# Kernel tuning notes

Measured on AMD Instinct MI355X. Metric: run time of the kernel, lower is better.

The kernel has to match this reference:

```python
import jax, jax.numpy as jnp
import numpy as np

N_NODES = 100000
N_EDGES = 1600000
HID = 64
BN_EPS = 1e-5


def _glorot(key, shape):
    fan_in, fan_out = shape[0], shape[1]
    lim = np.sqrt(6.0 / (fan_in + fan_out))
    return jax.random.uniform(key, shape, jnp.float32, -lim, lim)


def setup_inputs() -> dict:
    key = jax.random.key(0)
    ks = jax.random.split(key, 16)
    inp = {
        "x": jax.random.normal(ks[0], (N_NODES, HID), jnp.float32),
        "edge_index": jax.random.randint(ks[1], (2, N_EDGES), 0, N_NODES, jnp.int64),
        "edge_attr": jax.random.normal(ks[2], (N_EDGES,), jnp.float32),
    }
    # per-layer GIN MLP params: Linear(in,hid) -> BN(hid) -> ReLU -> Linear(hid,out)
    for i in range(2):
        inp[f"W1_{i}"] = _glorot(ks[3 + 5 * i], (HID, HID))
        inp[f"b1_{i}"] = jnp.zeros((HID,), jnp.float32)
        inp[f"gamma_{i}"] = jnp.ones((HID,), jnp.float32)
        inp[f"beta_{i}"] = jnp.zeros((HID,), jnp.float32)
        inp[f"W2_{i}"] = _glorot(ks[4 + 5 * i], (HID, HID))
        inp[f"b2_{i}"] = jnp.zeros((HID,), jnp.float32)
    inp["Wjk"] = _glorot(ks[14], (3 * HID, HID))
    inp["bjk"] = jnp.zeros((HID,), jnp.float32)
    return inp


def _gin_conv(x, src, dst, W1, b1, gamma, beta, W2, b2):
    # GIN aggregation: (1 + eps) * x + sum_{j->i} x_j, eps = 0
    agg = jax.ops.segment_sum(x[src], dst, num_segments=N_NODES)  # [N, d]
    h = (x + agg) @ W1 + b1
    # BatchNorm1d over node dimension (training-style batch statistics)
    mean = jnp.mean(h, axis=0)
    var = jnp.var(h, axis=0)
    h = gamma * (h - mean) * jax.lax.rsqrt(var + BN_EPS) + beta
    h = jax.nn.relu(h)
    return h @ W2 + b2


def reference(x, edge_index, edge_attr,
              W1_0, b1_0, gamma_0, beta_0, W2_0, b2_0,
              W1_1, b1_1, gamma_1, beta_1, W2_1, b2_1,
              Wjk, bjk):
    # edge_attr is accepted but ignored (torch_geometric GINConv does not use it)
    src, dst = edge_index[0], edge_index[1]
    xs = [x]
    h = x
    params = [(W1_0, b1_0, gamma_0, beta_0, W2_0, b2_0),
              (W1_1, b1_1, gamma_1, beta_1, W2_1, b2_1)]
    for p in params:
        h = _gin_conv(h, src, dst, *p)
        h = jax.nn.relu(h)  # dropout p=0.0 is identity
        xs.append(h)
    return jnp.concatenate(xs, axis=-1) @ Wjk + bjk
```

## Files before the change

### kernel.cpp

```cpp
#include <hip/hip_runtime.h>

#define N_NODES 100000
#define N_EDGES 1600000
#define HID 64
#define BN_EPS 1e-5f

#define GATHER_BLOCKS (N_NODES / 32)

#define ROW_TILES (N_NODES / 16)
#define TPW1 4
#define G1_BLOCKS ((ROW_TILES + 4*TPW1 - 1) / (4*TPW1))
#define TPW2 2
#define G2_BLOCKS ((ROW_TILES + 4*TPW2 - 1) / (4*TPW2))

#define NB 391
#define MS_BLOCKS 1000
#define MS_EPB (N_EDGES / MS_BLOCKS)
#define MS_CNT (NB * MS_BLOCKS)
#define GS_CHUNK 512
#define GS_BLOCKS ((MS_CNT + GS_CHUNK - 1) / GS_CHUNK)

typedef __bf16 bf16x8 __attribute__((ext_vector_type(8)));
typedef float  f32x4  __attribute__((ext_vector_type(4)));
typedef unsigned short u16x8 __attribute__((ext_vector_type(8)));

__device__ __forceinline__ float bf2f(unsigned short u) {
    return __uint_as_float(((unsigned)u) << 16);
}
__device__ __forceinline__ unsigned short f2bf_rne(float f) {
    unsigned u = __float_as_uint(f);
    u += 0x7FFFu + ((u >> 16) & 1u);
    return (unsigned short)(u >> 16);
}

__global__ __launch_bounds__(256) void cvt_bf16_kernel(
        const float* __restrict__ in, unsigned short* __restrict__ out) {
    size_t i = ((size_t)blockIdx.x * 256 + threadIdx.x) * 8;
    if (i >= (size_t)N_NODES * HID) return;
    float4 a = *reinterpret_cast<const float4*>(in + i);
    float4 b = *reinterpret_cast<const float4*>(in + i + 4);
    ushort4 w0 = make_ushort4(f2bf_rne(a.x), f2bf_rne(a.y), f2bf_rne(a.z), f2bf_rne(a.w));
    ushort4 w1 = make_ushort4(f2bf_rne(b.x), f2bf_rne(b.y), f2bf_rne(b.z), f2bf_rne(b.w));
    *reinterpret_cast<ushort4*>(out + i) = w0;
    *reinterpret_cast<ushort4*>(out + i + 4) = w1;
}

__global__ __launch_bounds__(256) void wtrans_all_kernel(
        const float* __restrict__ Wjk,
        const float* __restrict__ W1_0, const float* __restrict__ W2_0,
        const float* __restrict__ W1_1, const float* __restrict__ W2_1,
        unsigned short* __restrict__ wjk_t,
        unsigned short* __restrict__ w1t_0, unsigned short* __restrict__ w2t_0,
        unsigned short* __restrict__ w1t_1, unsigned short* __restrict__ w2t_1) {
    int i = blockIdx.x * 256 + threadIdx.x;
    if (i < 12288) {
        int c = i / 192, k = i - c * 192;
        wjk_t[i] = f2bf_rne(Wjk[k * 64 + c]);
    } else if (i < 12288 + 16384) {
        int r = i - 12288;
        int which = r >> 12, rem = r & 4095;
        int c = rem >> 6, k = rem & 63;
        const float* W = (which == 0) ? W1_0 : (which == 1) ? W2_0
                       : (which == 2) ? W1_1 : W2_1;
        unsigned short* Wt = (which == 0) ? w1t_0 : (which == 1) ? w2t_0
                           : (which == 2) ? w1t_1 : w2t_1;
        Wt[rem] = f2bf_rne(W[k * 64 + c]);
    }
}

__global__ __launch_bounds__(256) void msplit_hist_kernel(
        const int* __restrict__ dst, int* __restrict__ cnt) {
    __shared__ int h[NB];
    for (int i = threadIdx.x; i < NB; i += 256) h[i] = 0;
    __syncthreads();
    const int e0 = blockIdx.x * MS_EPB;
    for (int e = e0 + threadIdx.x; e < e0 + MS_EPB; e += 256)
        atomicAdd(&h[dst[e] >> 8], 1);
    __syncthreads();
    for (int i = threadIdx.x; i < NB; i += 256)
        cnt[i * MS_BLOCKS + blockIdx.x] = h[i];
}

__global__ __launch_bounds__(256) void scan_partial_g(
        const int* __restrict__ in, int* __restrict__ out,
        int* __restrict__ bsums, int n) {
    __shared__ int sd[256];
    int t = threadIdx.x;
    int base = blockIdx.x * GS_CHUNK;
    int i0 = base + 2 * t, i1 = i0 + 1;
    int d0 = (i0 < n) ? in[i0] : 0;
    int d1 = (i1 < n) ? in[i1] : 0;
    sd[t] = d0 + d1;
    __syncthreads();
    for (int o = 1; o < 256; o <<= 1) {
        int v = (t >= o) ? sd[t - o] : 0;
        __syncthreads();
        sd[t] += v;
        __syncthreads();
    }
    int excl = sd[t] - (d0 + d1);
    if (i0 < n) out[i0] = excl;
    if (i1 < n) out[i1] = excl + d0;
    if (t == 255) bsums[blockIdx.x] = sd[255];
}

__global__ __launch_bounds__(256) void scan_bsums_kernel(int* __restrict__ bsums, int nb) {
    __shared__ int sd[256];
    int t = threadIdx.x;
    int v[4]; int s = 0;
#pragma unroll
    for (int k = 0; k < 4; ++k) {
        int i = t * 4 + k;
        v[k] = (i < nb) ? bsums[i] : 0;
        s += v[k];
    }
    sd[t] = s;
    __syncthreads();
    for (int o = 1; o < 256; o <<= 1) {
        int u = (t >= o) ? sd[t - o] : 0;
        __syncthreads();
        sd[t] += u;
        __syncthreads();
    }
    int run = sd[t] - s;
#pragma unroll
    for (int k = 0; k < 4; ++k) {
        int i = t * 4 + k;
        if (i < nb) bsums[i] = run;
        run += v[k];
    }
}

__global__ __launch_bounds__(256) void scan_addback_g(
        int* __restrict__ out, const int* __restrict__ bsums, int n, int total) {
    int t = threadIdx.x;
    int b = bsums[blockIdx.x];
    int base = blockIdx.x * GS_CHUNK;
    int i0 = base + 2 * t, i1 = i0 + 1;
    if (i0 < n) out[i0] += b;
    if (i1 < n) out[i1] += b;
    if (blockIdx.x == 0 && t == 0) out[n] = total;
}

__global__ __launch_bounds__(256) void msplit_scatter_kernel(
        const int* __restrict__ src, const int* __restrict__ dst,
        const int* __restrict__ psum, int* __restrict__ bucketed) {
    __shared__ int cur[NB];
    for (int i = threadIdx.x; i < NB; i += 256)
        cur[i] = psum[i * MS_BLOCKS + blockIdx.x];
    __syncthreads();
    const int e0 = blockIdx.x * MS_EPB;
    for (int e = e0 + threadIdx.x; e < e0 + MS_EPB; e += 256) {
        int d = dst[e];
        int p = atomicAdd(&cur[d >> 8], 1);
        bucketed[p] = (src[e] << 8) | (d & 255);
    }
}

__global__ __launch_bounds__(256) void bucket_csr_kernel(
        const int* __restrict__ bucketed, const int* __restrict__ psum,
        int* __restrict__ off, int* __restrict__ eidx) {
    const int j = blockIdx.x;
    const int t = threadIdx.x;
    __shared__ int deg[256];
    __shared__ int sd[256];
    __shared__ int base_s, size_s;
    if (t == 0) {
        int b = psum[j * MS_BLOCKS];
        int nxt = (j == NB - 1) ? N_EDGES : psum[(j + 1) * MS_BLOCKS];
        base_s = b; size_s = nxt - b;
    }
    deg[t] = 0;
    __syncthreads();
    const int base = base_s, size = size_s;
    const int nlo = j << 8;
    for (int i = t; i < size; i += 256)
        atomicAdd(&deg[(unsigned)bucketed[base + i] & 255u], 1);
    __syncthreads();
    int d0 = deg[t];
    sd[t] = d0;
    __syncthreads();
    for (int o = 1; o < 256; o <<= 1) {
        int v = (t >= o) ? sd[t - o] : 0;
        __syncthreads();
        sd[t] += v;
        __syncthreads();
    }
    int excl = sd[t] - d0;
    int g0 = nlo + t;
    if (g0 <= N_NODES) off[g0] = base + excl;
    __syncthreads();
    deg[t] = excl;
    __syncthreads();
    for (int i = t; i < size; i += 256) {
        unsigned e = (unsigned)bucketed[base + i];
        int p = atomicAdd(&deg[e & 255u], 1);
        eidx[base + p] = (int)(e >> 8);
    }
}

__global__ __launch_bounds__(256) void gather_kernel(
        const unsigned short* __restrict__ xb, const int* __restrict__ off,
        const int* __restrict__ eidx, unsigned short* __restrict__ aggb) {
    const int lane = threadIdx.x & 63;
    const int g    = lane >> 3;
    const int col  = (lane & 7) << 3;
    const int w    = threadIdx.x >> 6;
    const int n = blockIdx.x * 32 + w * 8 + g;

    const int beg = off[n], end = off[n + 1];
    bf16x8 s8 = *reinterpret_cast<const bf16x8*>(xb + (size_t)n * HID + col);
    float acc[8];
#pragma unroll
    for (int i = 0; i < 8; ++i) acc[i] = (float)s8[i];

    int j = beg;
    for (; j + 2 <= end; j += 2) {
        int s0 = eidx[j], s1 = eidx[j + 1];
        bf16x8 r0 = *reinterpret_cast<const bf16x8*>(xb + (size_t)s0 * HID + col);
        bf16x8 r1 = *reinterpret_cast<const bf16x8*>(xb + (size_t)s1 * HID + col);
#pragma unroll
        for (int i = 0; i < 8; ++i) acc[i] += (float)r0[i] + (float)r1[i];
    }
    if (j < end) {
        int s0 = eidx[j];
        bf16x8 r0 = *reinterpret_cast<const bf16x8*>(xb + (size_t)s0 * HID + col);
#pragma unroll
        for (int i = 0; i < 8; ++i) acc[i] += (float)r0[i];
    }

    u16x8 o;
#pragma unroll
    for (int i = 0; i < 8; ++i) o[i] = f2bf_rne(acc[i]);
    *reinterpret_cast<u16x8*>(aggb + (size_t)n * HID + col) = o;
}

__global__ __launch_bounds__(256) void gemm1_mfma_kernel(
        const unsigned short* __restrict__ aggb, const unsigned short* __restrict__ W1t,
        const float* __restrict__ bias, unsigned short* __restrict__ hb,
        float* __restrict__ stats_partial) {
    const int lane = threadIdx.x & 63;
    const int l15 = lane & 15, lhi = lane >> 4;
    const int w = threadIdx.x >> 6;

    bf16x8 bfrag[2][4];
    float bs[4];
#pragma unroll
    for (int f = 0; f < 4; ++f) {
        const unsigned short* wp = W1t + (size_t)(f * 16 + l15) * 64 + lhi * 8;
        bfrag[0][f] = *reinterpret_cast<const bf16x8*>(wp);
        bfrag[1][f] = *reinterpret_cast<const bf16x8*>(wp + 32);
        bs[f] = bias[f * 16 + l15];
    }

    float ssum[4] = {0.f, 0.f, 0.f, 0.f}, ssq[4] = {0.f, 0.f, 0.f, 0.f};

    const int tile0 = (blockIdx.x * 4 + w) * TPW1;
#pragma unroll
    for (int tt = 0; tt < TPW1; ++tt) {
        const int tile = tile0 + tt;
        if (tile < ROW_TILES) {
            const int r0 = tile * 16;
            const size_t arow = (size_t)(r0 + l15) * 64 + lhi * 8;
            bf16x8 a0 = *reinterpret_cast<const bf16x8*>(aggb + arow);
            bf16x8 a1 = *reinterpret_cast<const bf16x8*>(aggb + arow + 32);
            f32x4 acc[4];
#pragma unroll
            for (int f = 0; f < 4; ++f) acc[f] = (f32x4){bs[f], bs[f], bs[f], bs[f]};
#pragma unroll
            for (int f = 0; f < 4; ++f) {
                acc[f] = __builtin_amdgcn_mfma_f32_16x16x32_bf16(a0, bfrag[0][f], acc[f], 0, 0, 0);
                acc[f] = __builtin_amdgcn_mfma_f32_16x16x32_bf16(a1, bfrag[1][f], acc[f], 0, 0, 0);
            }
#pragma unroll
            for (int f = 0; f < 4; ++f)
#pragma unroll
                for (int i = 0; i < 4; ++i) {
                    hb[(size_t)(r0 + lhi * 4 + i) * 64 + f * 16 + l15] = f2bf_rne(acc[f][i]);
                    ssum[f] += acc[f][i];
                    ssq[f]  += acc[f][i] * acc[f][i];
                }
        }
    }

    __shared__ float red[2][4][256];
#pragma unroll
    for (int f = 0; f < 4; ++f) {
        red[0][f][threadIdx.x] = ssum[f];
        red[1][f][threadIdx.x] = ssq[f];
    }
    __syncthreads();
    if (threadIdx.x < 64) {
        int c = threadIdx.x, f = c >> 4, p = c & 15;
        float s = 0.f, q = 0.f;
#pragma unroll
        for (int u = 0; u < 16; ++u) {
            int t = (u >> 2) * 64 + (u & 3) * 16 + p;
            s += red[0][f][t];
            q += red[1][f][t];
        }
        stats_partial[(size_t)blockIdx.x * 128 + c]      = s;
        stats_partial[(size_t)blockIdx.x * 128 + 64 + c] = q;
    }
}

__global__ __launch_bounds__(256) void bn_gemm_mfma_kernel(
        const unsigned short* __restrict__ hb, const unsigned short* __restrict__ W2t,
        const float* __restrict__ bias, const float* __restrict__ scale,
        const float* __restrict__ shift, unsigned short* __restrict__ outb) {
    const int lane = threadIdx.x & 63;
    const int l15 = lane & 15, lhi = lane >> 4;
    const int w = threadIdx.x >> 6;

    bf16x8 bfrag[2][4];
    float bs[4];
#pragma unroll
    for (int f = 0; f < 4; ++f) {
        const unsigned short* wp = W2t + (size_t)(f * 16 + l15) * 64 + lhi * 8;
        bfrag[0][f] = *reinterpret_cast<const bf16x8*>(wp);
        bfrag[1][f] = *reinterpret_cast<const bf16x8*>(wp + 32);
        bs[f] = bias[f * 16 + l15];
    }
    float sc[2][8], sh[2][8];
#pragma unroll
    for (int t = 0; t < 2; ++t)
#pragma unroll
        for (int j = 0; j < 8; ++j) {
            int k = t * 32 + lhi * 8 + j;
            sc[t][j] = scale[k];
            sh[t][j] = shift[k];
        }

    const int tile0 = (blockIdx.x * 4 + w) * TPW2;
#pragma unroll
    for (int tt = 0; tt < TPW2; ++tt) {
        const int tile = tile0 + tt;
        if (tile >= ROW_TILES) return;
        const int r0 = tile * 16;
        f32x4 acc[4];
#pragma unroll
        for (int f = 0; f < 4; ++f) acc[f] = (f32x4){bs[f], bs[f], bs[f], bs[f]};
#pragma unroll
        for (int t = 0; t < 2; ++t) {
            const unsigned short* hp = hb + (size_t)(r0 + l15) * 64 + t * 32 + lhi * 8;
            bf16x8 raw = *reinterpret_cast<const bf16x8*>(hp);
            bf16x8 a;
#pragma unroll
            for (int j = 0; j < 8; ++j)
                a[j] = (__bf16)fmaxf(fmaf(sc[t][j], (float)raw[j], sh[t][j]), 0.f);
#pragma unroll
            for (int f = 0; f < 4; ++f)
                acc[f] = __builtin_amdgcn_mfma_f32_16x16x32_bf16(a, bfrag[t][f], acc[f], 0, 0, 0);
        }
#pragma unroll
        for (int f = 0; f < 4; ++f)
#pragma unroll
            for (int i = 0; i < 4; ++i)
                outb[(size_t)(r0 + lhi * 4 + i) * 64 + f * 16 + l15] =
                    f2bf_rne(fmaxf(acc[f][i], 0.f));
    }
}

__global__ __launch_bounds__(256) void jumphead_mfma_kernel(
        const unsigned short* __restrict__ xb, const unsigned short* __restrict__ h1b,
        const unsigned short* __restrict__ h2b, const unsigned short* __restrict__ Wt,
        const float* __restrict__ bjk, float* __restrict__ out) {
    const int lane = threadIdx.x & 63;
    const int l15 = lane & 15, lhi = lane >> 4;
    const int w = threadIdx.x >> 6;

    bf16x8 bfrag[6][4];
    float bs[4];
#pragma unroll
    for (int f = 0; f < 4; ++f) {
        const unsigned short* wp = Wt + (size_t)(f * 16 + l15) * 192 + lhi * 8;
#pragma unroll
        for (int t = 0; t < 6; ++t)
            bfrag[t][f] = *reinterpret_cast<const bf16x8*>(wp + t * 32);
        bs[f] = bjk[f * 16 + l15];
    }

    const int tile0 = (blockIdx.x * 4 + w) * TPW2;
#pragma unroll
    for (int tt = 0; tt < TPW2; ++tt) {
        const int tile = tile0 + tt;
        if (tile >= ROW_TILES) return;
        const int r0 = tile * 16;
        const size_t arow = (size_t)(r0 + l15) * 64 + lhi * 8;
        bf16x8 a0 = *reinterpret_cast<const bf16x8*>(xb + arow);
        bf16x8 a1 = *reinterpret_cast<const bf16x8*>(xb + arow + 32);
        bf16x8 a2 = *reinterpret_cast<const bf16x8*>(h1b + arow);
        bf16x8 a3 = *reinterpret_cast<const bf16x8*>(h1b + arow + 32);
        bf16x8 a4 = *reinterpret_cast<const bf16x8*>(h2b + arow);
        bf16x8 a5 = *reinterpret_cast<const bf16x8*>(h2b + arow + 32);
        f32x4 acc[4];
#pragma unroll
        for (int f = 0; f < 4; ++f) acc[f] = (f32x4){bs[f], bs[f], bs[f], bs[f]};
#pragma unroll
        for (int f = 0; f < 4; ++f) {
            acc[f] = __builtin_amdgcn_mfma_f32_16x16x32_bf16(a0, bfrag[0][f], acc[f], 0, 0, 0);
            acc[f] = __builtin_amdgcn_mfma_f32_16x16x32_bf16(a1, bfrag[1][f], acc[f], 0, 0, 0);
            acc[f] = __builtin_amdgcn_mfma_f32_16x16x32_bf16(a2, bfrag[2][f], acc[f], 0, 0, 0);
            acc[f] = __builtin_amdgcn_mfma_f32_16x16x32_bf16(a3, bfrag[3][f], acc[f], 0, 0, 0);
            acc[f] = __builtin_amdgcn_mfma_f32_16x16x32_bf16(a4, bfrag[4][f], acc[f], 0, 0, 0);
            acc[f] = __builtin_amdgcn_mfma_f32_16x16x32_bf16(a5, bfrag[5][f], acc[f], 0, 0, 0);
        }
#pragma unroll
        for (int f = 0; f < 4; ++f)
#pragma unroll
            for (int i = 0; i < 4; ++i)
                out[(size_t)(r0 + lhi * 4 + i) * 64 + f * 16 + l15] = acc[f][i];
    }
}

__global__ __launch_bounds__(1024) void bn_finalize_kernel(
        const float* __restrict__ stats_partial, int nblocks,
        const float* __restrict__ gamma, const float* __restrict__ beta,
        float* __restrict__ scale, float* __restrict__ shift) {
    __shared__ float red[2][1024];
    const int t = threadIdx.x;
    const int c = t & 63;
    const int chunk = t >> 6;
    float s = 0.f, q = 0.f;
    for (int b = chunk; b < nblocks; b += 16) {
        s += stats_partial[(size_t)b * 128 + c];
        q += stats_partial[(size_t)b * 128 + 64 + c];
    }
    red[0][t] = s;
    red[1][t] = q;
    __syncthreads();
    if (chunk == 0) {
        float ss = 0.f, qq = 0.f;
#pragma unroll
        for (int k = 0; k < 16; ++k) {
            ss += red[0][k * 64 + c];
            qq += red[1][k * 64 + c];
        }
        float mean = ss / (float)N_NODES;
        float var  = qq / (float)N_NODES - mean * mean;
        float scl  = gamma[c] * rsqrtf(var + BN_EPS);
        scale[c] = scl;
        shift[c] = beta[c] - mean * scl;
    }
}

extern "C" void kernel_launch(void* const* d_in, const int* in_sizes, int n_in,
                              void* d_out, int out_size, void* d_ws, size_t ws_size,
                              hipStream_t stream) {
    const float* x    = (const float*)d_in[0];
    const int*   ei   = (const int*)d_in[1];
    const int*   src  = ei;
    const int*   dst  = ei + N_EDGES;
    const float* W1_0 = (const float*)d_in[3];
    const float* b1_0 = (const float*)d_in[4];
    const float* g_0  = (const float*)d_in[5];
    const float* be_0 = (const float*)d_in[6];
    const float* W2_0 = (const float*)d_in[7];
    const float* b2_0 = (const float*)d_in[8];
    const float* W1_1 = (const float*)d_in[9];
    const float* b1_1 = (const float*)d_in[10];
    const float* g_1  = (const float*)d_in[11];
    const float* be_1 = (const float*)d_in[12];
    const float* W2_1 = (const float*)d_in[13];
    const float* b2_1 = (const float*)d_in[14];
    const float* Wjk  = (const float*)d_in[15];
    const float* bjk  = (const float*)d_in[16];

    const size_t FEAT = (size_t)N_NODES * HID;

    unsigned short* aggb = (unsigned short*)d_ws;
    unsigned short* hb   = aggb + FEAT;
    unsigned short* xb   = hb + FEAT;
    unsigned short* h1b  = xb + FEAT;
    unsigned short* h2b  = h1b + FEAT;
    float* stats = (float*)(h2b + FEAT);
    float* scale = stats + (size_t)G1_BLOCKS * 128;
    float* shift = scale + 64;
    int*   off   = (int*)(shift + 64);
    int*   eidx  = off + N_NODES + 2;
    int*   cnt   = eidx + N_EDGES;
    int*   psum  = cnt + MS_CNT;
    int*   bsums = psum + MS_CNT + 2;
    unsigned short* wjk_t = (unsigned short*)(bsums + 1024);
    unsigned short* w2t_0 = wjk_t + 64 * 192;
    unsigned short* w2t_1 = w2t_0 + 64 * 64;
    unsigned short* w1t_0 = w2t_1 + 64 * 64;
    unsigned short* w1t_1 = w1t_0 + 64 * 64;
    int*   bucketed = (int*)h2b;
    float* out   = (float*)d_out;

    cvt_bf16_kernel<<<(int)(FEAT / 8 / 256), 256, 0, stream>>>(x, xb);
    wtrans_all_kernel<<<(12288 + 16384 + 255) / 256, 256, 0, stream>>>(
        Wjk, W1_0, W2_0, W1_1, W2_1, wjk_t, w1t_0, w2t_0, w1t_1, w2t_1);

    msplit_hist_kernel<<<MS_BLOCKS, 256, 0, stream>>>(dst, cnt);
    scan_partial_g<<<GS_BLOCKS, 256, 0, stream>>>(cnt, psum, bsums, MS_CNT);
    scan_bsums_kernel<<<1, 256, 0, stream>>>(bsums, GS_BLOCKS);
    scan_addback_g<<<GS_BLOCKS, 256, 0, stream>>>(psum, bsums, MS_CNT, N_EDGES);
    msplit_scatter_kernel<<<MS_BLOCKS, 256, 0, stream>>>(src, dst, psum, bucketed);
    bucket_csr_kernel<<<NB, 256, 0, stream>>>(bucketed, psum, off, eidx);

    gather_kernel<<<GATHER_BLOCKS, 256, 0, stream>>>(xb, off, eidx, aggb);
    gemm1_mfma_kernel<<<G1_BLOCKS, 256, 0, stream>>>(aggb, w1t_0, b1_0, hb, stats);
    bn_finalize_kernel<<<1, 1024, 0, stream>>>(stats, G1_BLOCKS, g_0, be_0, scale, shift);
    bn_gemm_mfma_kernel<<<G2_BLOCKS, 256, 0, stream>>>(hb, w2t_0, b2_0, scale, shift, h1b);

    gather_kernel<<<GATHER_BLOCKS, 256, 0, stream>>>(h1b, off, eidx, aggb);
    gemm1_mfma_kernel<<<G1_BLOCKS, 256, 0, stream>>>(aggb, w1t_1, b1_1, hb, stats);
    bn_finalize_kernel<<<1, 1024, 0, stream>>>(stats, G1_BLOCKS, g_1, be_1, scale, shift);
    bn_gemm_mfma_kernel<<<G2_BLOCKS, 256, 0, stream>>>(hb, w2t_1, b2_1, scale, shift, h2b);

    jumphead_mfma_kernel<<<G2_BLOCKS, 256, 0, stream>>>(
        xb, h1b, h2b, wjk_t, bjk, out);
}
```

Baseline: 204.0 us.

## Merge prep kernels, fuse layer-2 MLP tail into jump head, widen gather unroll

Three setup kernels (x to bf16 conversion, weight transposes, destination histogram) are merged into one launch that picks its role by block index. The second-layer BN+ReLU+W2 GEMM is fused into the jumping-knowledge head, with h2 staged per tile through padded LDS instead of written to and read back from global memory. The gather loop is unrolled to four neighbors per iteration to put more loads in flight. These cut launch overhead and one global round trip of h2, at the cost of more registers in the fused kernel, which may lower occupancy.

```diff
diff --git a/kernel.cpp b/kernel.cpp
--- a/kernel.cpp
+++ b/kernel.cpp
@@ -20,6 +20,10 @@
 #define GS_CHUNK 512
 #define GS_BLOCKS ((MS_CNT + GS_CHUNK - 1) / GS_CHUNK)
 
+#define CVT_B 3125
+#define WT_B 112
+#define PREP_BLOCKS (CVT_B + WT_B + MS_BLOCKS)
+
 typedef __bf16 bf16x8 __attribute__((ext_vector_type(8)));
 typedef float  f32x4  __attribute__((ext_vector_type(4)));
 typedef unsigned short u16x8 __attribute__((ext_vector_type(8)));
@@ -33,52 +37,51 @@
     return (unsigned short)(u >> 16);
 }
 
-__global__ __launch_bounds__(256) void cvt_bf16_kernel(
-        const float* __restrict__ in, unsigned short* __restrict__ out) {
-    size_t i = ((size_t)blockIdx.x * 256 + threadIdx.x) * 8;
-    if (i >= (size_t)N_NODES * HID) return;
-    float4 a = *reinterpret_cast<const float4*>(in + i);
-    float4 b = *reinterpret_cast<const float4*>(in + i + 4);
-    ushort4 w0 = make_ushort4(f2bf_rne(a.x), f2bf_rne(a.y), f2bf_rne(a.z), f2bf_rne(a.w));
-    ushort4 w1 = make_ushort4(f2bf_rne(b.x), f2bf_rne(b.y), f2bf_rne(b.z), f2bf_rne(b.w));
-    *reinterpret_cast<ushort4*>(out + i) = w0;
-    *reinterpret_cast<ushort4*>(out + i + 4) = w1;
-}
-
-__global__ __launch_bounds__(256) void wtrans_all_kernel(
+__global__ __launch_bounds__(256) void prep_kernel(
+        const float* __restrict__ x, unsigned short* __restrict__ xb,
         const float* __restrict__ Wjk,
         const float* __restrict__ W1_0, const float* __restrict__ W2_0,
         const float* __restrict__ W1_1, const float* __restrict__ W2_1,
         unsigned short* __restrict__ wjk_t,
         unsigned short* __restrict__ w1t_0, unsigned short* __restrict__ w2t_0,
-        unsigned short* __restrict__ w1t_1, unsigned short* __restrict__ w2t_1) {
-    int i = blockIdx.x * 256 + threadIdx.x;
-    if (i < 12288) {
-        int c = i / 192, k = i - c * 192;
-        wjk_t[i] = f2bf_rne(Wjk[k * 64 + c]);
-    } else if (i < 12288 + 16384) {
-        int r = i - 12288;
-        int which = r >> 12, rem = r & 4095;
-        int c = rem >> 6, k = rem & 63;
-        const float* W = (which == 0) ? W1_0 : (which == 1) ? W2_0
-                       : (which == 2) ? W1_1 : W2_1;
-        unsigned short* Wt = (which == 0) ? w1t_0 : (which == 1) ? w2t_0
-                           : (which == 2) ? w1t_1 : w2t_1;
-        Wt[rem] = f2bf_rne(W[k * 64 + c]);
-    }
-}
-
-__global__ __launch_bounds__(256) void msplit_hist_kernel(
+        unsigned short* __restrict__ w1t_1, unsigned short* __restrict__ w2t_1,
         const int* __restrict__ dst, int* __restrict__ cnt) {
     __shared__ int h[NB];
-    for (int i = threadIdx.x; i < NB; i += 256) h[i] = 0;
-    __syncthreads();
-    const int e0 = blockIdx.x * MS_EPB;
-    for (int e = e0 + threadIdx.x; e < e0 + MS_EPB; e += 256)
-        atomicAdd(&h[dst[e] >> 8], 1);
-    __syncthreads();
-    for (int i = threadIdx.x; i < NB; i += 256)
-        cnt[i * MS_BLOCKS + blockIdx.x] = h[i];
+    const int b = blockIdx.x;
+    if (b < CVT_B) {
+        size_t i = ((size_t)b * 256 + threadIdx.x) * 8;
+        float4 a = *reinterpret_cast<const float4*>(x + i);
+        float4 c = *reinterpret_cast<const float4*>(x + i + 4);
+        ushort4 w0 = make_ushort4(f2bf_rne(a.x), f2bf_rne(a.y), f2bf_rne(a.z), f2bf_rne(a.w));
+        ushort4 w1 = make_ushort4(f2bf_rne(c.x), f2bf_rne(c.y), f2bf_rne(c.z), f2bf_rne(c.w));
+        *reinterpret_cast<ushort4*>(xb + i) = w0;
+        *reinterpret_cast<ushort4*>(xb + i + 4) = w1;
+    } else if (b < CVT_B + WT_B) {
+        int i = (b - CVT_B) * 256 + threadIdx.x;
+        if (i < 12288) {
+            int c = i / 192, k = i - c * 192;
+            wjk_t[i] = f2bf_rne(Wjk[k * 64 + c]);
+        } else {
+            int r = i - 12288;
+            int which = r >> 12, rem = r & 4095;
+            int c = rem >> 6, k = rem & 63;
+            const float* W = (which == 0) ? W1_0 : (which == 1) ? W2_0
+                           : (which == 2) ? W1_1 : W2_1;
+            unsigned short* Wt = (which == 0) ? w1t_0 : (which == 1) ? w2t_0
+                               : (which == 2) ? w1t_1 : w2t_1;
+            Wt[rem] = f2bf_rne(W[k * 64 + c]);
+        }
+    } else {
+        const int hb = b - CVT_B - WT_B;
+        for (int i = threadIdx.x; i < NB; i += 256) h[i] = 0;
+        __syncthreads();
+        const int e0 = hb * MS_EPB;
+        for (int e = e0 + threadIdx.x; e < e0 + MS_EPB; e += 256)
+            atomicAdd(&h[dst[e] >> 8], 1);
+        __syncthreads();
+        for (int i = threadIdx.x; i < NB; i += 256)
+            cnt[i * MS_BLOCKS + hb] = h[i];
+    }
 }
 
 __global__ __launch_bounds__(256) void scan_partial_g(
@@ -215,14 +218,17 @@
     for (int i = 0; i < 8; ++i) acc[i] = (float)s8[i];
 
     int j = beg;
-    for (; j + 2 <= end; j += 2) {
-        int s0 = eidx[j], s1 = eidx[j + 1];
+    for (; j + 4 <= end; j += 4) {
+        int s0 = eidx[j], s1 = eidx[j + 1], s2 = eidx[j + 2], s3 = eidx[j + 3];
         bf16x8 r0 = *reinterpret_cast<const bf16x8*>(xb + (size_t)s0 * HID + col);
         bf16x8 r1 = *reinterpret_cast<const bf16x8*>(xb + (size_t)s1 * HID + col);
-#pragma unroll
-        for (int i = 0; i < 8; ++i) acc[i] += (float)r0[i] + (float)r1[i];
-    }
-    if (j < end) {
+        bf16x8 r2 = *reinterpret_cast<const bf16x8*>(xb + (size_t)s2 * HID + col);
+        bf16x8 r3 = *reinterpret_cast<const bf16x8*>(xb + (size_t)s3 * HID + col);
+#pragma unroll
+        for (int i = 0; i < 8; ++i)
+            acc[i] += ((float)r0[i] + (float)r1[i]) + ((float)r2[i] + (float)r3[i]);
+    }
+    for (; j < end; ++j) {
         int s0 = eidx[j];
         bf16x8 r0 = *reinterpret_cast<const bf16x8*>(xb + (size_t)s0 * HID + col);
 #pragma unroll
@@ -361,23 +367,46 @@
     }
 }
 
-__global__ __launch_bounds__(256) void jumphead_mfma_kernel(
+#define LT_STRIDE 88
+__global__ __launch_bounds__(256) void bn_gemm_jumphead_kernel(
+        const unsigned short* __restrict__ hb, const unsigned short* __restrict__ W2t,
+        const float* __restrict__ bias2, const float* __restrict__ scale,
+        const float* __restrict__ shift,
         const unsigned short* __restrict__ xb, const unsigned short* __restrict__ h1b,
-        const unsigned short* __restrict__ h2b, const unsigned short* __restrict__ Wt,
-        const float* __restrict__ bjk, float* __restrict__ out) {
+        const unsigned short* __restrict__ Wt, const float* __restrict__ bjk,
+        float* __restrict__ out) {
+    __shared__ unsigned short lt[4][16 * LT_STRIDE];
     const int lane = threadIdx.x & 63;
     const int l15 = lane & 15, lhi = lane >> 4;
     const int w = threadIdx.x >> 6;
 
-    bf16x8 bfrag[6][4];
-    float bs[4];
+    bf16x8 b2frag[2][4];
+    float bs2[4];
+#pragma unroll
+    for (int f = 0; f < 4; ++f) {
+        const unsigned short* wp = W2t + (size_t)(f * 16 + l15) * 64 + lhi * 8;
+        b2frag[0][f] = *reinterpret_cast<const bf16x8*>(wp);
+        b2frag[1][f] = *reinterpret_cast<const bf16x8*>(wp + 32);
+        bs2[f] = bias2[f * 16 + l15];
+    }
+    float sc[2][8], sh[2][8];
+#pragma unroll
+    for (int t = 0; t < 2; ++t)
+#pragma unroll
+        for (int j = 0; j < 8; ++j) {
+            int k = t * 32 + lhi * 8 + j;
+            sc[t][j] = scale[k];
+            sh[t][j] = shift[k];
+        }
+    bf16x8 bjfrag[6][4];
+    float bsj[4];
 #pragma unroll
     for (int f = 0; f < 4; ++f) {
         const unsigned short* wp = Wt + (size_t)(f * 16 + l15) * 192 + lhi * 8;
 #pragma unroll
         for (int t = 0; t < 6; ++t)
-            bfrag[t][f] = *reinterpret_cast<const bf16x8*>(wp + t * 32);
-        bs[f] = bjk[f * 16 + l15];
+            bjfrag[t][f] = *reinterpret_cast<const bf16x8*>(wp + t * 32);
+        bsj[f] = bjk[f * 16 + l15];
     }
 
     const int tile0 = (blockIdx.x * 4 + w) * TPW2;
@@ -386,30 +415,53 @@
         const int tile = tile0 + tt;
         if (tile >= ROW_TILES) return;
         const int r0 = tile * 16;
+
+        f32x4 acc2[4];
+#pragma unroll
+        for (int f = 0; f < 4; ++f) acc2[f] = (f32x4){bs2[f], bs2[f], bs2[f], bs2[f]};
+#pragma unroll
+        for (int t = 0; t < 2; ++t) {
+            const unsigned short* hp = hb + (size_t)(r0 + l15) * 64 + t * 32 + lhi * 8;
+            bf16x8 raw = *reinterpret_cast<const bf16x8*>(hp);
+            bf16x8 a;
+#pragma unroll
+            for (int j = 0; j < 8; ++j)
+                a[j] = (__bf16)fmaxf(fmaf(sc[t][j], (float)raw[j], sh[t][j]), 0.f);
+#pragma unroll
+            for (int f = 0; f < 4; ++f)
+                acc2[f] = __builtin_amdgcn_mfma_f32_16x16x32_bf16(a, b2frag[t][f], acc2[f], 0, 0, 0);
+        }
+#pragma unroll
+        for (int f = 0; f < 4; ++f)
+#pragma unroll
+            for (int i = 0; i < 4; ++i)
+                lt[w][(lhi * 4 + i) * LT_STRIDE + f * 16 + l15] =
+                    f2bf_rne(fmaxf(acc2[f][i], 0.f));
+        bf16x8 a4 = *reinterpret_cast<const bf16x8*>(&lt[w][l15 * LT_STRIDE + lhi * 8]);
+        bf16x8 a5 = *reinterpret_cast<const bf16x8*>(&lt[w][l15 * LT_STRIDE + 32 + lhi * 8]);
+
         const size_t arow = (size_t)(r0 + l15) * 64 + lhi * 8;
         bf16x8 a0 = *reinterpret_cast<const bf16x8*>(xb + arow);
         bf16x8 a1 = *reinterpret_cast<const bf16x8*>(xb + arow + 32);
         bf16x8 a2 = *reinterpret_cast<const bf16x8*>(h1b + arow);
         bf16x8 a3 = *reinterpret_cast<const bf16x8*>(h1b + arow + 32);
-        bf16x8 a4 = *reinterpret_cast<const bf16x8*>(h2b + arow);
-        bf16x8 a5 = *reinterpret_cast<const bf16x8*>(h2b + arow + 32);
-        f32x4 acc[4];
-#pragma unroll
-        for (int f = 0; f < 4; ++f) acc[f] = (f32x4){bs[f], bs[f], bs[f], bs[f]};
+        f32x4 accj[4];
+#pragma unroll
+        for (int f = 0; f < 4; ++f) accj[f] = (f32x4){bsj[f], bsj[f], bsj[f], bsj[f]};
 #pragma unroll
         for (int f = 0; f < 4; ++f) {
-            acc[f] = __builtin_amdgcn_mfma_f32_16x16x32_bf16(a0, bfrag[0][f], acc[f], 0, 0, 0);
-            acc[f] = __builtin_amdgcn_mfma_f32_16x16x32_bf16(a1, bfrag[1][f], acc[f], 0, 0, 0);
-            acc[f] = __builtin_amdgcn_mfma_f32_16x16x32_bf16(a2, bfrag[2][f], acc[f], 0, 0, 0);
-            acc[f] = __builtin_amdgcn_mfma_f32_16x16x32_bf16(a3, bfrag[3][f], acc[f], 0, 0, 0);
-            acc[f] = __builtin_amdgcn_mfma_f32_16x16x32_bf16(a4, bfrag[4][f], acc[f], 0, 0, 0);
-            acc[f] = __builtin_amdgcn_mfma_f32_16x16x32_bf16(a5, bfrag[5][f], acc[f], 0, 0, 0);
+            accj[f] = __builtin_amdgcn_mfma_f32_16x16x32_bf16(a0, bjfrag[0][f], accj[f], 0, 0, 0);
+            accj[f] = __builtin_amdgcn_mfma_f32_16x16x32_bf16(a1, bjfrag[1][f], accj[f], 0, 0, 0);
+            accj[f] = __builtin_amdgcn_mfma_f32_16x16x32_bf16(a2, bjfrag[2][f], accj[f], 0, 0, 0);
+            accj[f] = __builtin_amdgcn_mfma_f32_16x16x32_bf16(a3, bjfrag[3][f], accj[f], 0, 0, 0);
+            accj[f] = __builtin_amdgcn_mfma_f32_16x16x32_bf16(a4, bjfrag[4][f], accj[f], 0, 0, 0);
+            accj[f] = __builtin_amdgcn_mfma_f32_16x16x32_bf16(a5, bjfrag[5][f], accj[f], 0, 0, 0);
         }
 #pragma unroll
         for (int f = 0; f < 4; ++f)
 #pragma unroll
             for (int i = 0; i < 4; ++i)
-                out[(size_t)(r0 + lhi * 4 + i) * 64 + f * 16 + l15] = acc[f][i];
+                out[(size_t)(r0 + lhi * 4 + i) * 64 + f * 16 + l15] = accj[f][i];
     }
 }
 
@@ -472,8 +524,8 @@
     unsigned short* hb   = aggb + FEAT;
     unsigned short* xb   = hb + FEAT;
     unsigned short* h1b  = xb + FEAT;
-    unsigned short* h2b  = h1b + FEAT;
-    float* stats = (float*)(h2b + FEAT);
+    int*   bucketed = (int*)(h1b + FEAT);
+    float* stats = (float*)(bucketed + N_EDGES);
     float* scale = stats + (size_t)G1_BLOCKS * 128;
     float* shift = scale + 64;
     int*   off   = (int*)(shift + 64);
@@ -486,14 +538,12 @@
     unsigned short* w2t_1 = w2t_0 + 64 * 64;
     unsigned short* w1t_0 = w2t_1 + 64 * 64;
     unsigned short* w1t_1 = w1t_0 + 64 * 64;
-    int*   bucketed = (int*)h2b;
     float* out   = (float*)d_out;
 
-    cvt_bf16_kernel<<<(int)(FEAT / 8 / 256), 256, 0, stream>>>(x, xb);
-    wtrans_all_kernel<<<(12288 + 16384 + 255) / 256, 256, 0, stream>>>(
-        Wjk, W1_0, W2_0, W1_1, W2_1, wjk_t, w1t_0, w2t_0, w1t_1, w2t_1);
-
-    msplit_hist_kernel<<<MS_BLOCKS, 256, 0, stream>>>(dst, cnt);
+    prep_kernel<<<PREP_BLOCKS, 256, 0, stream>>>(
+        x, xb, Wjk, W1_0, W2_0, W1_1, W2_1,
+        wjk_t, w1t_0, w2t_0, w1t_1, w2t_1, dst, cnt);
+
     scan_partial_g<<<GS_BLOCKS, 256, 0, stream>>>(cnt, psum, bsums, MS_CNT);
     scan_bsums_kernel<<<1, 256, 0, stream>>>(bsums, GS_BLOCKS);
     scan_addback_g<<<GS_BLOCKS, 256, 0, stream>>>(psum, bsums, MS_CNT, N_EDGES);
@@ -508,8 +558,6 @@
     gather_kernel<<<GATHER_BLOCKS, 256, 0, stream>>>(h1b, off, eidx, aggb);
     gemm1_mfma_kernel<<<G1_BLOCKS, 256, 0, stream>>>(aggb, w1t_1, b1_1, hb, stats);
     bn_finalize_kernel<<<1, 1024, 0, stream>>>(stats, G1_BLOCKS, g_1, be_1, scale, shift);
-    bn_gemm_mfma_kernel<<<G2_BLOCKS, 256, 0, stream>>>(hb, w2t_1, b2_1, scale, shift, h2b);
-
-    jumphead_mfma_kernel<<<G2_BLOCKS, 256, 0, stream>>>(
-        xb, h1b, h2b, wjk_t, bjk, out);
-}
+    bn_gemm_jumphead_kernel<<<G2_BLOCKS, 256, 0, stream>>>(
+        hb, w2t_1, b2_1, scale, shift, xb, h1b, wjk_t, bjk, out);
+}
```

After: 190.3 us. -6.7%, faster.
